# Kernel tuning notes

Hardware: AMD Instinct MI355X
Metric: run time of the kernel (lower is better)

## Reference

```python
import jax, jax.numpy as jnp
import numpy as np

IN_F = 4096
OUT_F = 4096
RANK = 16
NUM_SLOTS = 32
ALPHA = 1.0


def setup_inputs() -> dict:
    key = jax.random.key(0)
    k_x, k_w, k_b, k_a, k_bm, k_idx = jax.random.split(key, 6)
    x = jax.random.normal(k_x, (8, 2048, IN_F), dtype=jnp.float32)
    weight = jax.random.normal(k_w, (OUT_F, IN_F), dtype=jnp.float32) * (1.0 / np.sqrt(IN_F))
    bias = jax.random.normal(k_b, (OUT_F,), dtype=jnp.float32) * 0.01
    lora_A = jax.random.normal(k_a, (NUM_SLOTS, IN_F, RANK), dtype=jnp.float32) * 1e-4
    lora_B = jax.random.normal(k_bm, (NUM_SLOTS, RANK, OUT_F), dtype=jnp.float32) * 1e-4
    lora_indices = jax.random.randint(k_idx, (8,), 0, NUM_SLOTS)
    return {"x": x, "weight": weight, "bias": bias, "lora_A": lora_A,
            "lora_B": lora_B, "lora_indices": lora_indices}


def reference(x, weight, bias, lora_A, lora_B, lora_indices):
    # base linear: x @ W.T + b
    out = jnp.einsum('bsd,od->bso', x, weight) + bias
    # per-sample LoRA slot gather + low-rank bmm chain
    chosen_A = lora_A[lora_indices]          # [B, in, r]
    chosen_B = lora_B[lora_indices]          # [B, r, out]
    inter = jnp.einsum('bsd,bdr->bsr', x, chosen_A)       # [B, S, r]
    out_lora = jnp.einsum('bsr,bro->bso', inter, chosen_B)  # [B, S, out]
    return out + ALPHA * out_lora
```

## Files before the change

kernel.cpp:

```cpp
#include <hip/hip_runtime.h>
#include <hip/hip_bf16.h>


#define M_TOT 16384
#define K_TOT 4096
#define N_TOT 4096
#define RANK 16
#define NT 128

typedef __attribute__((ext_vector_type(8))) short bf16x8;
typedef __attribute__((ext_vector_type(4))) float f32x4;

__device__ __forceinline__ unsigned short f2bf(float f) {
  unsigned int u = __builtin_bit_cast(unsigned int, f);
  u += 0x7fffu + ((u >> 16) & 1u);
  return (unsigned short)(u >> 16);
}

__global__ void cvt_bf16_kernel(const float* __restrict__ src,
                                unsigned short* __restrict__ dst, int n4) {
  int i = blockIdx.x * blockDim.x + threadIdx.x;
  const int stride = gridDim.x * blockDim.x;
  for (; i < n4; i += stride) {
    const float4 v = reinterpret_cast<const float4*>(src)[i];
    ushort4 o;
    o.x = f2bf(v.x); o.y = f2bf(v.y); o.z = f2bf(v.z); o.w = f2bf(v.w);
    reinterpret_cast<ushort4*>(dst)[i] = o;
  }
}

__global__ __launch_bounds__(256) void lora_inter_mfma_kernel(
    const unsigned short* __restrict__ xb,
    const float* __restrict__ loraA,
    const int* __restrict__ idx,
    float* __restrict__ inter) {
  const int lane = threadIdx.x & 63;
  const int wv = threadIdx.x >> 6;
  const int m0 = blockIdx.x * 64 + wv * 16;
  const int slot = idx[m0 >> 11];
  const int q = lane >> 4;
  const int c = lane & 15;
  const unsigned short* __restrict__ xrow = xb + (size_t)(m0 + c) * K_TOT + q * 8;
  const float* __restrict__ Abase = loraA + (size_t)slot * K_TOT * RANK + c;

  f32x4 acc = (f32x4){0.f, 0.f, 0.f, 0.f};
#pragma unroll 4
  for (int kt = 0; kt < K_TOT; kt += 32) {
    const bf16x8 af = *reinterpret_cast<const bf16x8*>(xrow + kt);
    const float* __restrict__ Ak = Abase + (size_t)(kt + q * 8) * RANK;
    bf16x8 bfr;
#pragma unroll
    for (int j = 0; j < 8; ++j) bfr[j] = (short)f2bf(Ak[(size_t)j * RANK]);
    acc = __builtin_amdgcn_mfma_f32_16x16x32_bf16(af, bfr, acc, 0, 0, 0);
  }
#pragma unroll
  for (int i = 0; i < 4; ++i)
    inter[(size_t)(m0 + q * 4 + i) * RANK + c] = acc[i];
}

__device__ __forceinline__ void gload16(const void* g, void* l) {
  __builtin_amdgcn_global_load_lds(
      (const __attribute__((address_space(1))) unsigned int*)g,
      (__attribute__((address_space(3))) unsigned int*)l, 16, 0, 0);
}

#define GBARRIER() asm volatile("s_barrier" ::: "memory")
#define WAIT_LGKM0()                                   \
  do {                                                 \
    asm volatile("s_waitcnt lgkmcnt(0)" ::: "memory"); \
    __builtin_amdgcn_sched_barrier(0);                 \
  } while (0)

__global__ __launch_bounds__(512, 2) void gemm_fused_kernel(
    const unsigned short* __restrict__ xb,
    const unsigned short* __restrict__ wb,
    const float* __restrict__ bias,
    const float* __restrict__ inter,
    const float* __restrict__ loraB,
    const int* __restrict__ idx,
    float* __restrict__ out) {
  __shared__ unsigned short lds[4][16384];
  char* ldsB = (char*)&lds[0][0];

  const int tid = threadIdx.x;
  const int lane = tid & 63;
  const int wv = tid >> 6;
  const int wr = wv >> 2;
  const int wc = wv & 3;

  const int bid = ((blockIdx.x & 7) << 7) | (blockIdx.x >> 3);
  const int m0 = (bid >> 4) << 8;
  const int n0 = (bid & 15) << 8;

  const int srow = tid >> 2;
  const int sslot = (tid & 3) ^ ((srow >> 1) & 3);
  const unsigned short* xs0 = xb + (size_t)(m0 + srow) * K_TOT + sslot * 8;
  const unsigned short* xs1 = xs0 + (size_t)128 * K_TOT;
  const unsigned short* ws0 = wb + (size_t)(n0 + srow) * K_TOT + sslot * 8;
  const unsigned short* ws1 = ws0 + (size_t)128 * K_TOT;
  const int stgoff = wv << 10;

#define STAGE_A(t)                                                  \
  do {                                                              \
    const int _bo = (((t) & 3) << 15);                              \
    gload16(xs0 + (size_t)(t) * 32, ldsB + _bo + stgoff);           \
    gload16(xs1 + (size_t)(t) * 32, ldsB + _bo + 8192 + stgoff);    \
  } while (0)
#define STAGE_B(t)                                                  \
  do {                                                              \
    const int _bo = (((t) & 3) << 15);                              \
    gload16(ws0 + (size_t)(t) * 32, ldsB + _bo + 16384 + stgoff);   \
    gload16(ws1 + (size_t)(t) * 32, ldsB + _bo + 24576 + stgoff);   \
  } while (0)

  const int rl = lane & 15;
  const int q = lane >> 4;
  const int pslot = ((q ^ ((rl >> 1) & 3)) << 4);
  const int aoff = (wr * 128 + rl) * 64 + pslot;
  const int boff = 16384 + (wc * 64 + rl) * 64 + pslot;

  f32x4 acc[8][4];
#pragma unroll
  for (int i = 0; i < 8; ++i)
#pragma unroll
    for (int j = 0; j < 4; ++j) acc[i][j] = (f32x4){0.f, 0.f, 0.f, 0.f};

  STAGE_A(0); STAGE_B(0);
  STAGE_A(1); STAGE_B(1);
  STAGE_A(2); STAGE_B(2);
  asm volatile("s_waitcnt vmcnt(8)" ::: "memory");
  GBARRIER();

#pragma unroll 1
  for (int t = 0; t < NT; ++t) {
    const char* Ab = ldsB + ((t & 3) << 15) + aoff;
    const char* Bb = ldsB + ((t & 3) << 15) + boff;
    bf16x8 afrag[4], bfrag[4];

#pragma unroll
    for (int nf = 0; nf < 4; ++nf)
      bfrag[nf] = *reinterpret_cast<const bf16x8*>(Bb + nf * 1024);
#pragma unroll
    for (int mf = 0; mf < 4; ++mf)
      afrag[mf] = *reinterpret_cast<const bf16x8*>(Ab + mf * 1024);
    if (t < NT - 3) STAGE_A(t + 3);
    GBARRIER();
    WAIT_LGKM0();
    __builtin_amdgcn_s_setprio(1);
#pragma unroll
    for (int mf = 0; mf < 4; ++mf)
#pragma unroll
      for (int nf = 0; nf < 4; ++nf)
        acc[mf][nf] = __builtin_amdgcn_mfma_f32_16x16x32_bf16(
            afrag[mf], bfrag[nf], acc[mf][nf], 0, 0, 0);
    __builtin_amdgcn_s_setprio(0);
    GBARRIER();

#pragma unroll
    for (int mf = 0; mf < 4; ++mf)
      afrag[mf] = *reinterpret_cast<const bf16x8*>(Ab + (4 + mf) * 1024);
    if (t < NT - 3) STAGE_B(t + 3);
    GBARRIER();
    WAIT_LGKM0();
    __builtin_amdgcn_s_setprio(1);
#pragma unroll
    for (int mf = 0; mf < 4; ++mf)
#pragma unroll
      for (int nf = 0; nf < 4; ++nf)
        acc[4 + mf][nf] = __builtin_amdgcn_mfma_f32_16x16x32_bf16(
            afrag[mf], bfrag[nf], acc[4 + mf][nf], 0, 0, 0);
    __builtin_amdgcn_s_setprio(0);
    if (t < NT - 3) {
      asm volatile("s_waitcnt vmcnt(8)" ::: "memory");
    } else {
      asm volatile("s_waitcnt vmcnt(0)" ::: "memory");
    }
    GBARRIER();
  }

  const int slot = idx[m0 >> 11];
  const float* __restrict__ Bmat = loraB + (size_t)slot * RANK * N_TOT;
  const int gn0 = n0 + wc * 64 + rl;

  float bcv[4][RANK];
  float bv[4];
#pragma unroll
  for (int nf = 0; nf < 4; ++nf) {
    const int gn = gn0 + nf * 16;
    bv[nf] = bias[gn];
#pragma unroll
    for (int p = 0; p < RANK; ++p) bcv[nf][p] = Bmat[(size_t)p * N_TOT + gn];
  }
#pragma unroll
  for (int mf = 0; mf < 8; ++mf) {
    const int gmb = m0 + wr * 128 + mf * 16 + (q << 2);
#pragma unroll
    for (int r = 0; r < 4; ++r) {
      const int gm = gmb + r;
      const float4* ivp = reinterpret_cast<const float4*>(inter + (size_t)gm * RANK);
      const float4 iv0 = ivp[0], iv1 = ivp[1], iv2 = ivp[2], iv3 = ivp[3];
      float* orow = out + (size_t)gm * N_TOT;
#pragma unroll
      for (int nf = 0; nf < 4; ++nf) {
        const float lora =
            iv0.x * bcv[nf][0]  + iv0.y * bcv[nf][1]  + iv0.z * bcv[nf][2]  + iv0.w * bcv[nf][3] +
            iv1.x * bcv[nf][4]  + iv1.y * bcv[nf][5]  + iv1.z * bcv[nf][6]  + iv1.w * bcv[nf][7] +
            iv2.x * bcv[nf][8]  + iv2.y * bcv[nf][9]  + iv2.z * bcv[nf][10] + iv2.w * bcv[nf][11] +
            iv3.x * bcv[nf][12] + iv3.y * bcv[nf][13] + iv3.z * bcv[nf][14] + iv3.w * bcv[nf][15];
        orow[gn0 + nf * 16] = acc[mf][nf][r] + bv[nf] + lora;
      }
    }
  }
#undef STAGE_A
#undef STAGE_B
}

extern "C" void kernel_launch(void* const* d_in, const int* in_sizes, int n_in,
                              void* d_out, int out_size, void* d_ws, size_t ws_size,
                              hipStream_t stream) {
  const float* x     = (const float*)d_in[0];
  const float* w     = (const float*)d_in[1];
  const float* bias  = (const float*)d_in[2];
  const float* loraA = (const float*)d_in[3];
  const float* loraB = (const float*)d_in[4];
  const int*   idx   = (const int*)d_in[5];
  float* out = (float*)d_out;

  char* ws = (char*)d_ws;
  unsigned short* xb   = (unsigned short*)ws;
  unsigned short* wbuf = (unsigned short*)(ws + 134217728);
  float* inter = (float*)(ws + 134217728 + 33554432);

  cvt_bf16_kernel<<<2048, 256, 0, stream>>>(x, xb, M_TOT * K_TOT / 4);
  cvt_bf16_kernel<<<1024, 256, 0, stream>>>(w, wbuf, N_TOT * K_TOT / 4);
  lora_inter_mfma_kernel<<<M_TOT / 64, 256, 0, stream>>>(xb, loraA, idx, inter);
  gemm_fused_kernel<<<(M_TOT / 256) * (N_TOT / 256), 512, 0, stream>>>(
      xb, wbuf, bias, inter, loraB, idx, out);
}
```

Baseline: 692.4 us.

## Collapse two-phase K-loop into single phase with one barrier per tile

```diff
diff --git a/kernel.cpp b/kernel.cpp
--- a/kernel.cpp
+++ b/kernel.cpp
@@ -65,11 +65,6 @@
 }
 
 #define GBARRIER() asm volatile("s_barrier" ::: "memory")
-#define WAIT_LGKM0()                                   \
-  do {                                                 \
-    asm volatile("s_waitcnt lgkmcnt(0)" ::: "memory"); \
-    __builtin_amdgcn_sched_barrier(0);                 \
-  } while (0)
 
 __global__ __launch_bounds__(512, 2) void gemm_fused_kernel(
     const unsigned short* __restrict__ xb,
@@ -100,15 +95,11 @@
   const unsigned short* ws1 = ws0 + (size_t)128 * K_TOT;
   const int stgoff = wv << 10;
 
-#define STAGE_A(t)                                                  \
+#define STAGE_T(t)                                                  \
   do {                                                              \
     const int _bo = (((t) & 3) << 15);                              \
     gload16(xs0 + (size_t)(t) * 32, ldsB + _bo + stgoff);           \
     gload16(xs1 + (size_t)(t) * 32, ldsB + _bo + 8192 + stgoff);    \
-  } while (0)
-#define STAGE_B(t)                                                  \
-  do {                                                              \
-    const int _bo = (((t) & 3) << 15);                              \
     gload16(ws0 + (size_t)(t) * 32, ldsB + _bo + 16384 + stgoff);   \
     gload16(ws1 + (size_t)(t) * 32, ldsB + _bo + 24576 + stgoff);   \
   } while (0)
@@ -125,9 +116,7 @@
 #pragma unroll
     for (int j = 0; j < 4; ++j) acc[i][j] = (f32x4){0.f, 0.f, 0.f, 0.f};
 
-  STAGE_A(0); STAGE_B(0);
-  STAGE_A(1); STAGE_B(1);
-  STAGE_A(2); STAGE_B(2);
+  STAGE_T(0); STAGE_T(1); STAGE_T(2);
   asm volatile("s_waitcnt vmcnt(8)" ::: "memory");
   GBARRIER();
 
@@ -135,43 +124,34 @@
   for (int t = 0; t < NT; ++t) {
     const char* Ab = ldsB + ((t & 3) << 15) + aoff;
     const char* Bb = ldsB + ((t & 3) << 15) + boff;
-    bf16x8 afrag[4], bfrag[4];
-
+
+    bf16x8 bfrag[4], afrag[8];
 #pragma unroll
     for (int nf = 0; nf < 4; ++nf)
       bfrag[nf] = *reinterpret_cast<const bf16x8*>(Bb + nf * 1024);
 #pragma unroll
-    for (int mf = 0; mf < 4; ++mf)
+    for (int mf = 0; mf < 8; ++mf)
       afrag[mf] = *reinterpret_cast<const bf16x8*>(Ab + mf * 1024);
-    if (t < NT - 3) STAGE_A(t + 3);
-    GBARRIER();
-    WAIT_LGKM0();
+    if (t < NT - 3) STAGE_T(t + 3);
+
+    asm volatile("s_waitcnt lgkmcnt(0)" ::: "memory");
+    __builtin_amdgcn_sched_barrier(0);
     __builtin_amdgcn_s_setprio(1);
 #pragma unroll
-    for (int mf = 0; mf < 4; ++mf)
+    for (int mf = 0; mf < 8; ++mf)
 #pragma unroll
       for (int nf = 0; nf < 4; ++nf)
         acc[mf][nf] = __builtin_amdgcn_mfma_f32_16x16x32_bf16(
             afrag[mf], bfrag[nf], acc[mf][nf], 0, 0, 0);
     __builtin_amdgcn_s_setprio(0);
-    GBARRIER();
-
-#pragma unroll
-    for (int mf = 0; mf < 4; ++mf)
-      afrag[mf] = *reinterpret_cast<const bf16x8*>(Ab + (4 + mf) * 1024);
-    if (t < NT - 3) STAGE_B(t + 3);
-    GBARRIER();
-    WAIT_LGKM0();
-    __builtin_amdgcn_s_setprio(1);
-#pragma unroll
-    for (int mf = 0; mf < 4; ++mf)
-#pragma unroll
-      for (int nf = 0; nf < 4; ++nf)
-        acc[4 + mf][nf] = __builtin_amdgcn_mfma_f32_16x16x32_bf16(
-            afrag[mf], bfrag[nf], acc[4 + mf][nf], 0, 0, 0);
-    __builtin_amdgcn_s_setprio(0);
-    if (t < NT - 3) {
+    __builtin_amdgcn_sched_barrier(0);
+
+    if (t < NT - 4) {
       asm volatile("s_waitcnt vmcnt(8)" ::: "memory");
+    } else if (t == NT - 4) {
+      asm volatile("s_waitcnt vmcnt(8)" ::: "memory");
+    } else if (t == NT - 3) {
+      asm volatile("s_waitcnt vmcnt(4)" ::: "memory");
     } else {
       asm volatile("s_waitcnt vmcnt(0)" ::: "memory");
     }
@@ -211,8 +191,7 @@
       }
     }
   }
-#undef STAGE_A
-#undef STAGE_B
+#undef STAGE_T
 }
 
 extern "C" void kernel_launch(void* const* d_in, const int* in_sizes, int n_in,
```

Result: faster. 671.8 us (-3.0%).
